# Kernel optimization log

Hardware: AMD Instinct MI355X
Metric: run time of the kernel (lower is better)

Reference implementation:

```python
import jax, jax.numpy as jnp
import numpy as np

B, S, D = 1, 2048, 1024
NH, NKV, WS = 8, 2, 64
HD = D // NH  # 128
E, HDIM, TOPK = 16, 512, 2
FP16_MIN = -65504.0
EPS = 1e-6
AUX_COEFF = 1e-5


def rmsnorm(x, w):
    return x * jax.lax.rsqrt(jnp.mean(x * x, axis=-1, keepdims=True) + EPS) * w


def setup_inputs() -> dict:
    key = jax.random.key(0)
    ks = jax.random.split(key, 24)
    r = lambda k, shape, fan: jax.random.normal(k, shape, dtype=jnp.float32) * (1.0 / np.sqrt(fan))
    return {
        "x": jax.random.normal(ks[0], (B, S, D), dtype=jnp.float32),
        "norm1_w": jnp.ones((D,), jnp.float32),
        "wq": r(ks[1], (D, NH * HD), D), "bq": jnp.zeros((NH * HD,), jnp.float32),
        "wk": r(ks[2], (D, NKV * HD), D), "bk": jnp.zeros((NKV * HD,), jnp.float32),
        "wv": r(ks[3], (D, NKV * HD), D), "bv": jnp.zeros((NKV * HD,), jnp.float32),
        "wo": r(ks[4], (NH * HD, D), NH * HD), "bo": jnp.zeros((D,), jnp.float32),
        "sink_bias": jnp.zeros((), jnp.float32),
        "norm2_w": jnp.ones((D,), jnp.float32),
        "router_w": r(ks[5], (D, E), D), "router_b": jnp.zeros((E,), jnp.float32),
        "w1": r(ks[6], (E, D, HDIM), D), "b1": jnp.zeros((E, HDIM), jnp.float32),
        "w2": r(ks[7], (E, HDIM, D), HDIM), "b2": jnp.zeros((E, D), jnp.float32),
    }


def reference(x, norm1_w, wq, bq, wk, bk, wv, bv, wo, bo, sink_bias,
              norm2_w, router_w, router_b, w1, b1, w2, b2):
    # ---- sliding-window attention with sink softmax ----
    h = rmsnorm(x, norm1_w)
    q = (h @ wq + bq).reshape(B, S, NH, HD).transpose(0, 2, 1, 3)    # [B,NH,S,HD]
    k = (h @ wk + bk).reshape(B, S, NKV, HD).transpose(0, 2, 1, 3)   # [B,NKV,S,HD]
    v = (h @ wv + bv).reshape(B, S, NKV, HD).transpose(0, 2, 1, 3)
    k = jnp.repeat(k, NH // NKV, axis=1)  # GQA expand -> [B,NH,S,HD]
    v = jnp.repeat(v, NH // NKV, axis=1)
    scores = jnp.einsum('bhqd,bhkd->bhqk', q, k) / np.sqrt(HD)
    i = jnp.arange(S)[:, None]
    j = jnp.arange(S)[None, :]
    band = (i - j >= 0) & (i - j <= WS - 1)  # causal sliding window
    scores = jnp.where(band, scores, FP16_MIN)
    m = jnp.maximum(jnp.max(scores, axis=-1, keepdims=True), sink_bias)
    ew = jnp.exp(scores - m)
    denom = jnp.sum(ew, axis=-1, keepdims=True) + jnp.exp(sink_bias - m)
    attn = ew / denom
    out = jnp.einsum('bhqk,bhkd->bhqd', attn, v).transpose(0, 2, 1, 3).reshape(B, S, D)
    x = x + (out @ wo + bo)

    # ---- MoE FFN ----
    h2 = rmsnorm(x, norm2_w)
    xf = h2.reshape(-1, D)                                  # [N,D]
    logits = (xf @ router_w + router_b) / 0.1               # [N,E]
    top_v, top_i = jax.lax.top_k(logits, TOPK)              # [N,k]
    top_w = jax.nn.softmax(top_v, axis=-1)
    probs = jax.nn.softmax(logits, axis=-1)
    aux_loss = jnp.sum(jnp.sum(probs, axis=0) ** 2) / E * AUX_COEFF
    # combine weights per (token, expert)
    gate = jnp.sum(jax.nn.one_hot(top_i, E, dtype=xf.dtype) * top_w[..., None], axis=1)  # [N,E]
    hmid = jax.nn.silu(jnp.einsum('nd,edh->neh', xf, w1) + b1)   # [N,E,H]
    y = jnp.einsum('neh,ehd->ned', hmid, w2) + b2                # [N,E,D]
    ffn = jnp.einsum('ne,ned->nd', gate, y)
    x = x + ffn.reshape(B, S, D)
    return x, aux_loss
```

## Files before the change

### kernel.cpp

```cpp
#include <hip/hip_runtime.h>
#include <hip/hip_bf16.h>

#define S     2048
#define D     1024
#define NH    8
#define NKV   2
#define HD    128
#define WS_   64
#define E_    16
#define HDIM  512
#define TOPK  2
#define NTOK  S
#define NSLOT (S*TOPK)
#define QKV_M (D + 2*NKV*HD)
#define KOFF  D
#define VOFF  (D + NKV*HD)
#define QB    8
#define WROWS (QB + WS_ - 1)
#define KPITCH 73
#define VPADF  132

typedef __attribute__((ext_vector_type(8))) short bf16x8;
typedef __attribute__((ext_vector_type(4))) float floatx4;

__device__ inline short f2bf(float f) {
    __hip_bfloat16 b = __float2bfloat16(f);
    return *reinterpret_cast<short*>(&b);
}

__global__ __launch_bounds__(256) void tconv_all(
    const float* __restrict__ wq, const float* __restrict__ wk,
    const float* __restrict__ wv, const float* __restrict__ wo,
    const float* __restrict__ w1, const float* __restrict__ w2,
    const float* __restrict__ bq, const float* __restrict__ bk,
    const float* __restrict__ bv, const float* __restrict__ router_w,
    short* __restrict__ wqkvT, short* __restrict__ woT,
    short* __restrict__ w1T, short* __restrict__ w2T,
    float* __restrict__ bqkv, float* __restrict__ rwT)
{
    int id = blockIdx.x;
    if (id >= 18950) {
        int ky = id - 18950;
        int t = threadIdx.x;
        int r = t >> 4, c = t & 15;
        int k0 = ky * 32;
        rwT[c * D + k0 + r]      = router_w[(k0 + r) * E_ + c];
        rwT[c * D + k0 + r + 16] = router_w[(k0 + r + 16) * E_ + c];
        return;
    }
    if (id >= 18944) {
        int t = (id - 18944) * 256 + threadIdx.x;
        if (t < D) bqkv[t] = bq[t];
        else if (t < VOFF) bqkv[t] = bk[t - D];
        else bqkv[t] = bv[t - VOFF];
        return;
    }
    const float* in; short* outp; int K, M, mx, ky;
    if (id < 1024)      { in = wq; outp = wqkvT;                  K = D; M = D;   int l = id;        mx = l & 31; ky = l >> 5; }
    else if (id < 1280) { in = wk; outp = wqkvT + (size_t)KOFF*D; K = D; M = 256; int l = id - 1024; mx = l & 7;  ky = l >> 3; }
    else if (id < 1536) { in = wv; outp = wqkvT + (size_t)VOFF*D; K = D; M = 256; int l = id - 1280; mx = l & 7;  ky = l >> 3; }
    else if (id < 2560) { in = wo; outp = woT;                    K = D; M = D;   int l = id - 1536; mx = l & 31; ky = l >> 5; }
    else if (id < 10752){ int l = id - 2560;  int e = l >> 9; int r = l & 511;
                          in = w1 + (size_t)e * D * HDIM; outp = w1T + (size_t)e * D * HDIM;
                          K = D; M = HDIM; mx = r & 15; ky = r >> 4; }
    else                { int l = id - 10752; int e = l >> 9; int r = l & 511;
                          in = w2 + (size_t)e * D * HDIM; outp = w2T + (size_t)e * D * HDIM;
                          K = HDIM; M = D; mx = r & 31; ky = r >> 5; }
    __shared__ float tile[32][33];
    int t = threadIdx.x, r = t >> 3, c4 = (t & 7) * 4;
    int k0 = ky * 32, m0 = mx * 32;
    float4 v = *(const float4*)&in[(size_t)(k0 + r) * M + m0 + c4];
    tile[r][c4 + 0] = v.x; tile[r][c4 + 1] = v.y;
    tile[r][c4 + 2] = v.z; tile[r][c4 + 3] = v.w;
    __syncthreads();
    short4 o;
    o.x = f2bf(tile[c4 + 0][r]);
    o.y = f2bf(tile[c4 + 1][r]);
    o.z = f2bf(tile[c4 + 2][r]);
    o.w = f2bf(tile[c4 + 3][r]);
    *(short4*)&outp[(size_t)(m0 + r) * K + k0 + c4] = o;
}

__global__ __launch_bounds__(256) void rmsnorm_kernel(
    const float* __restrict__ x, const float* __restrict__ w,
    short* __restrict__ outb)
{
    int row = blockIdx.x, t = threadIdx.x;
    float4 v = ((const float4*)(x + (size_t)row * D))[t];
    float ss = v.x*v.x + v.y*v.y + v.z*v.z + v.w*v.w;
    #pragma unroll
    for (int off = 32; off; off >>= 1) ss += __shfl_xor(ss, off, 64);
    __shared__ float red[4];
    if ((t & 63) == 0) red[t >> 6] = ss;
    __syncthreads();
    float total = red[0] + red[1] + red[2] + red[3];
    float scale = rsqrtf(total * (1.0f / (float)D) + 1e-6f);
    float4 wv = ((const float4*)w)[t];
    short4 ob;
    ob.x = f2bf(v.x * scale * wv.x); ob.y = f2bf(v.y * scale * wv.y);
    ob.z = f2bf(v.z * scale * wv.z); ob.w = f2bf(v.w * scale * wv.w);
    ((short4*)(outb + (size_t)row * D))[t] = ob;
}

template <int V, int RT>
__global__ __launch_bounds__(256) void mgemm(
    const short* __restrict__ A, const short* __restrict__ Bt,
    const float* __restrict__ bias, float* __restrict__ C,
    short* __restrict__ Cb, const float* __restrict__ res, int K, int M,
    const int* __restrict__ offs, const float* __restrict__ tok_gate)
{
    int e = (V >= 2) ? blockIdx.z : 0;
    const short* Bte = (V >= 2) ? Bt + (size_t)e * M * K : Bt;
    const float* be  = (V >= 2) ? bias + (size_t)e * M : bias;

    int row_lo, row_hi;
    if (V >= 2) {
        row_lo = offs[e] + blockIdx.y * RT;
        row_hi = offs[e + 1];
        if (row_lo >= row_hi) return;
    } else {
        row_lo = blockIdx.y * RT;
        row_hi = 1 << 30;
    }
    int col0 = blockIdx.x * 64;

    __shared__ short As[RT * 40];
    __shared__ short Bs[64 * 40];

    int t = threadIdx.x;
    int arow, ak;
    if (RT == 128) { arow = t >> 1; ak = (t & 1) * 16; }
    else           { arow = t >> 2; ak = (t & 3) * 8;  }
    int brow = t >> 2, bk = (t & 3) * 8;

    int  agrow = row_lo + arow;
    bool aval  = (V < 2) || (agrow < row_hi);
    int  asrc  = aval ? agrow : row_lo;
    const short* aptr = A   + (size_t)asrc * K + ak;
    const short* bptr = Bte + (size_t)(col0 + brow) * K + bk;
    short* as_dst = &As[arow * 40 + ak];
    short* bs_dst = &Bs[brow * 40 + bk];

    int lane = t & 63, wave = t >> 6;
    constexpr int AI = RT / 32;
    int wm = (wave & 1) * (RT / 2), wn = (wave >> 1) * 32;
    int rin = lane & 15, quad = lane >> 4;

    floatx4 acc[AI][2];
    #pragma unroll
    for (int i = 0; i < AI; ++i)
        #pragma unroll
        for (int j = 0; j < 2; ++j)
            acc[i][j] = (floatx4){0.f, 0.f, 0.f, 0.f};

    float4 a0, a1, b0;
    a0 = *(const float4*)(aptr);
    if (RT == 128) a1 = *(const float4*)(aptr + 8);
    b0 = *(const float4*)(bptr);

    for (int k0 = 0; k0 < K; k0 += 32) {
        __syncthreads();
        *(float4*)(as_dst) = a0;
        if (RT == 128) *(float4*)(as_dst + 8) = a1;
        *(float4*)(bs_dst) = b0;
        __syncthreads();
        if (k0 + 32 < K) {
            a0 = *(const float4*)(aptr + k0 + 32);
            if (RT == 128) a1 = *(const float4*)(aptr + k0 + 40);
            b0 = *(const float4*)(bptr + k0 + 32);
        }
        bf16x8 af[AI], bfr[2];
        #pragma unroll
        for (int i = 0; i < AI; ++i)
            af[i] = *(const bf16x8*)&As[(wm + i * 16 + rin) * 40 + quad * 8];
        #pragma unroll
        for (int j = 0; j < 2; ++j)
            bfr[j] = *(const bf16x8*)&Bs[(wn + j * 16 + rin) * 40 + quad * 8];
        #pragma unroll
        for (int i = 0; i < AI; ++i)
            #pragma unroll
            for (int j = 0; j < 2; ++j)
                acc[i][j] = __builtin_amdgcn_mfma_f32_16x16x32_bf16(
                    af[i], bfr[j], acc[i][j], 0, 0, 0);
    }

    #pragma unroll
    for (int i = 0; i < AI; ++i) {
        #pragma unroll
        for (int j = 0; j < 2; ++j) {
            int cg = col0 + wn + j * 16 + rin;
            #pragma unroll
            for (int rr = 0; rr < 4; ++rr) {
                int rg = row_lo + wm + i * 16 + quad * 4 + rr;
                float val = acc[i][j][rr];
                if (V == 0) {
                    C[(size_t)rg * M + cg] = val + be[cg];
                } else if (V == 1) {
                    C[(size_t)rg * M + cg] = val + be[cg] + res[(size_t)rg * M + cg];
                } else if (V == 2) {
                    if (rg < row_hi) {
                        float vb_ = val + be[cg];
                        Cb[(size_t)rg * M + cg] = f2bf(vb_ / (1.f + __expf(-vb_)));
                    }
                } else {
                    if (rg < row_hi)
                        C[(size_t)rg * M + cg] = tok_gate[rg] * (val + be[cg]);
                }
            }
        }
    }
}

__global__ __launch_bounds__(256) void attn_kernel(
    const float* __restrict__ qkv, const float* __restrict__ sink_ptr,
    short* __restrict__ ao)
{
    __shared__ __align__(16) float KT[32 * KPITCH * 4];
    __shared__ __align__(16) float Vs[WROWS * VPADF];
    __shared__ __align__(16) float Ps4[4][64][4];

    int qblk = blockIdx.x;
    int kvh  = blockIdx.y;
    int q0   = qblk * QB;
    int jbase = q0 - (WS_ - 1);

    int t = threadIdx.x;
    int c4 = (t & 31) * 4, c4g = t & 31;
    for (int r = t >> 5; r < WROWS; r += 8) {
        int j = jbase + r;
        float4 kv4 = make_float4(0.f, 0.f, 0.f, 0.f);
        float4 vv4 = make_float4(0.f, 0.f, 0.f, 0.f);
        if (j >= 0) {
            kv4 = *(const float4*)(qkv + (size_t)j * QKV_M + KOFF + kvh * HD + c4);
            vv4 = *(const float4*)(qkv + (size_t)j * QKV_M + VOFF + kvh * HD + c4);
        }
        *(float4*)&KT[(c4g * KPITCH + r) * 4] = kv4;
        *(float4*)&Vs[r * VPADF + c4] = vv4;
    }
    __syncthreads();

    int lane = t & 63, wv = t >> 6;
    float sink = sink_ptr[0];
    const float rscale = 0.08838834764831845f;

    #pragma unroll
    for (int g = 0; g < 2; ++g) {
        int qi = wv * 2 + g;
        int i  = q0 + qi;
        bool valid = (jbase + qi + lane) >= 0;

        float sc[4] = {0.f, 0.f, 0.f, 0.f};
        const float* qbase = qkv + (size_t)i * QKV_M + (kvh * 4) * HD;
        #pragma unroll
        for (int c = 0; c < 32; ++c) {
            float4 kx = *(const float4*)&KT[(c * KPITCH + qi + lane) * 4];
            #pragma unroll
            for (int hh = 0; hh < 4; ++hh) {
                float4 q4 = *(const float4*)(qbase + hh * HD + c * 4);
                sc[hh] += q4.x*kx.x + q4.y*kx.y + q4.z*kx.z + q4.w*kx.w;
            }
        }

        float pn[4];
        #pragma unroll
        for (int hh = 0; hh < 4; ++hh) {
            float s = valid ? sc[hh] * rscale : -1e30f;
            float m = s;
            #pragma unroll
            for (int off = 32; off; off >>= 1) m = fmaxf(m, __shfl_xor(m, off, 64));
            float mf = fmaxf(m, sink);
            float p  = __expf(s - mf);
            float ds = p;
            #pragma unroll
            for (int off = 32; off; off >>= 1) ds += __shfl_xor(ds, off, 64);
            pn[hh] = p / (ds + __expf(sink - mf));
        }
        *(float4*)&Ps4[wv][lane][0] = make_float4(pn[0], pn[1], pn[2], pn[3]);

        float o0=0,o1=0,o2=0,o3=0,o4=0,o5=0,o6=0,o7=0;
        const float* vp = &Vs[qi * VPADF + 2 * lane];
        #pragma unroll
        for (int jj = 0; jj < 64; ++jj) {
            float4 p4 = *(const float4*)&Ps4[wv][jj][0];
            float2 vv = *(const float2*)(vp + jj * VPADF);
            o0 += p4.x * vv.x; o1 += p4.x * vv.y;
            o2 += p4.y * vv.x; o3 += p4.y * vv.y;
            o4 += p4.z * vv.x; o5 += p4.z * vv.y;
            o6 += p4.w * vv.x; o7 += p4.w * vv.y;
        }
        short2 r0; r0.x = f2bf(o0); r0.y = f2bf(o1);
        short2 r1; r1.x = f2bf(o2); r1.y = f2bf(o3);
        short2 r2; r2.x = f2bf(o4); r2.y = f2bf(o5);
        short2 r3; r3.x = f2bf(o6); r3.y = f2bf(o7);
        ((short2*)(ao + (size_t)i * D + (kvh * 4 + 0) * HD))[lane] = r0;
        ((short2*)(ao + (size_t)i * D + (kvh * 4 + 1) * HD))[lane] = r1;
        ((short2*)(ao + (size_t)i * D + (kvh * 4 + 2) * HD))[lane] = r2;
        ((short2*)(ao + (size_t)i * D + (kvh * 4 + 3) * HD))[lane] = r3;
    }
}

__global__ __launch_bounds__(256) void rms_router_kernel(
    const float* __restrict__ x1, const float* __restrict__ w,
    short* __restrict__ h2b, const float* __restrict__ rwT,
    const float* __restrict__ rb, float* __restrict__ probs,
    int* __restrict__ top_i, float* __restrict__ top_g)
{
    int tok = blockIdx.x, t = threadIdx.x;
    __shared__ float hrow[D];
    float4 v = ((const float4*)(x1 + (size_t)tok * D))[t];
    float ss = v.x*v.x + v.y*v.y + v.z*v.z + v.w*v.w;
    #pragma unroll
    for (int off = 32; off; off >>= 1) ss += __shfl_xor(ss, off, 64);
    __shared__ float red[4];
    if ((t & 63) == 0) red[t >> 6] = ss;
    __syncthreads();
    float total = red[0] + red[1] + red[2] + red[3];
    float scale = rsqrtf(total * (1.0f / (float)D) + 1e-6f);
    float4 wv = ((const float4*)w)[t];
    float4 o;
    o.x = v.x * scale * wv.x; o.y = v.y * scale * wv.y;
    o.z = v.z * scale * wv.z; o.w = v.w * scale * wv.w;
    ((float4*)hrow)[t] = o;
    short4 ob;
    ob.x = f2bf(o.x); ob.y = f2bf(o.y); ob.z = f2bf(o.z); ob.w = f2bf(o.w);
    ((short4*)(h2b + (size_t)tok * D))[t] = ob;
    __syncthreads();

    int e = t & 15, seg = t >> 4;
    const float4* rwp = (const float4*)(rwT + (size_t)e * D + seg * 64);
    const float4* hp  = (const float4*)(hrow + seg * 64);
    float part = 0.f;
    #pragma unroll
    for (int i = 0; i < 16; ++i) {
        float4 a = hp[i];
        float4 b = rwp[i];
        part += a.x * b.x; part += a.y * b.y;
        part += a.z * b.z; part += a.w * b.w;
    }
    __shared__ float lpart[256];
    lpart[t] = part;
    __syncthreads();
    __shared__ float logits[E_];
    if (t < E_) {
        float sl = 0.f;
        for (int sg = 0; sg < 16; ++sg) sl += lpart[sg * 16 + t];
        logits[t] = (sl + rb[t]) * 10.0f;
    }
    __syncthreads();
    __shared__ float sm[2];
    if (t == 0) {
        float mx = logits[0];
        for (int x = 1; x < E_; ++x) mx = fmaxf(mx, logits[x]);
        float ps = 0.f;
        for (int x = 0; x < E_; ++x) ps += __expf(logits[x] - mx);
        sm[0] = mx; sm[1] = ps;
        int i0 = 0; float v0 = logits[0];
        for (int x = 1; x < E_; ++x) if (logits[x] > v0) { v0 = logits[x]; i0 = x; }
        int i1 = -1; float v1 = -3.4e38f;
        for (int x = 0; x < E_; ++x) {
            if (x == i0) continue;
            if (logits[x] > v1) { v1 = logits[x]; i1 = x; }
        }
        float e1 = __expf(v1 - v0);
        float g0 = 1.f / (1.f + e1);
        float g1 = e1 * g0;
        top_i[tok * 2 + 0] = i0; top_g[tok * 2 + 0] = g0;
        top_i[tok * 2 + 1] = i1; top_g[tok * 2 + 1] = g1;
    }
    __syncthreads();
    if (t < E_) probs[tok * E_ + t] = __expf(logits[t] - sm[0]) / sm[1];
}

__global__ __launch_bounds__(256) void finalize_kernel(
    const float* __restrict__ probs, const int* __restrict__ top_i,
    int* __restrict__ offs, int* __restrict__ cursor,
    float* __restrict__ aux_out)
{
    __shared__ float csum[E_];
    __shared__ int hist[E_];
    int t = threadIdx.x;
    if (t < E_) { csum[t] = 0.f; hist[t] = 0; }
    __syncthreads();

    int c = t & 15, g = t >> 4;
    float part = 0.f;
    for (int i = 0; i < NTOK / 16; ++i)
        part += probs[(size_t)(i * 16 + g) * E_ + c];
    atomicAdd(&csum[c], part);

    int h = 0;
    for (int i = 0; i < NSLOT / 256; ++i) {
        int eidx = top_i[i * 256 + t];
        atomicAdd(&hist[eidx], 1);
    }
    (void)h;
    __syncthreads();

    if (t == 0) {
        int acc = 0;
        for (int e = 0; e < E_; ++e) { offs[e] = acc; cursor[e] = acc; acc += hist[e]; }
        offs[E_] = acc;
        float s = 0.f;
        for (int e = 0; e < E_; ++e) s += csum[e] * csum[e];
        *aux_out = s / (float)E_ * 1e-5f;
    }
}

__global__ __launch_bounds__(256) void scatter_kernel(
    const int* __restrict__ top_i, const float* __restrict__ top_g,
    int* __restrict__ cursor, int* __restrict__ tok_idx,
    float* __restrict__ tok_gate, int* __restrict__ slot_of)
{
    int tok = blockIdx.x * 256 + threadIdx.x;
    if (tok >= NTOK) return;
    for (int s = 0; s < TOPK; ++s) {
        int e = top_i[tok * 2 + s];
        int pos = atomicAdd(&cursor[e], 1);
        tok_idx[pos]  = tok;
        tok_gate[pos] = top_g[tok * 2 + s];
        slot_of[tok * 2 + s] = pos;
    }
}

__global__ __launch_bounds__(256) void gather_kernel(
    const short* __restrict__ h2b, const int* __restrict__ tok_idx,
    short* __restrict__ xg)
{
    int slot = blockIdx.x * 2 + (threadIdx.x >> 7);
    int c = (threadIdx.x & 127) * 8;
    int tok = tok_idx[slot];
    *(float4*)&xg[(size_t)slot * D + c] =
        *(const float4*)&h2b[(size_t)tok * D + c];
}

__global__ __launch_bounds__(256) void combine_kernel(
    const float* __restrict__ x1, const float* __restrict__ y,
    const int* __restrict__ slot_of, float* __restrict__ out)
{
    int tok = blockIdx.x, t = threadIdx.x;
    int s0 = slot_of[tok * 2], s1 = slot_of[tok * 2 + 1];
    float4 a = ((const float4*)(x1 + (size_t)tok * D))[t];
    float4 b = ((const float4*)(y + (size_t)s0 * D))[t];
    float4 c = ((const float4*)(y + (size_t)s1 * D))[t];
    float4 o;
    o.x = a.x + b.x + c.x; o.y = a.y + b.y + c.y;
    o.z = a.z + b.z + c.z; o.w = a.w + b.w + c.w;
    ((float4*)(out + (size_t)tok * D))[t] = o;
}

extern "C" void kernel_launch(void* const* d_in, const int* in_sizes, int n_in,
                              void* d_out, int out_size, void* d_ws, size_t ws_size,
                              hipStream_t stream)
{
    const float* x        = (const float*)d_in[0];
    const float* norm1_w  = (const float*)d_in[1];
    const float* wq       = (const float*)d_in[2];
    const float* bq       = (const float*)d_in[3];
    const float* wk       = (const float*)d_in[4];
    const float* bk       = (const float*)d_in[5];
    const float* wv       = (const float*)d_in[6];
    const float* bv       = (const float*)d_in[7];
    const float* wo       = (const float*)d_in[8];
    const float* bo       = (const float*)d_in[9];
    const float* sink     = (const float*)d_in[10];
    const float* norm2_w  = (const float*)d_in[11];
    const float* router_w = (const float*)d_in[12];
    const float* router_b = (const float*)d_in[13];
    const float* w1       = (const float*)d_in[14];
    const float* b1       = (const float*)d_in[15];
    const float* w2       = (const float*)d_in[16];
    const float* b2       = (const float*)d_in[17];
    float* out = (float*)d_out;

    char* w = (char*)d_ws;
    auto alloc = [&](size_t bytes) {
        char* p = w; w += (bytes + 255) & ~255ull; return p;
    };
    short* wqkvT = (short*)alloc((size_t)QKV_M * D * 2);
    short* woT   = (short*)alloc((size_t)D * D * 2);
    short* w1T   = (short*)alloc((size_t)E_ * HDIM * D * 2);
    short* w2T   = (short*)alloc((size_t)E_ * D * HDIM * 2);
    float* bqkv  = (float*)alloc(QKV_M * 4);
    float* rwT   = (float*)alloc((size_t)E_ * D * 4);
    short* h_bf  = (short*)alloc((size_t)S * D * 2);
    float* qkv   = (float*)alloc((size_t)S * QKV_M * 4);
    float* x1    = (float*)alloc((size_t)S * D * 4);
    short* h2b   = (short*)alloc((size_t)S * D * 2);
    short* xg    = (short*)alloc((size_t)NSLOT * D * 2);
    float* yslot = (float*)alloc((size_t)NSLOT * D * 4);
    float* probs = (float*)alloc((size_t)NTOK * E_ * 4);
    int*   offs     = (int*)alloc(17 * 4);
    int*   cursor   = (int*)alloc(16 * 4);
    int*   top_i    = (int*)alloc((size_t)NSLOT * 4);
    float* top_g    = (float*)alloc((size_t)NSLOT * 4);
    int*   tok_idx  = (int*)alloc((size_t)NSLOT * 4);
    float* tok_gate = (float*)alloc((size_t)NSLOT * 4);
    int*   slot_of  = (int*)alloc((size_t)NSLOT * 4);
    short* ao_bf = h_bf;
    short* hmid  = (short*)qkv;

    tconv_all<<<18982, 256, 0, stream>>>(wq, wk, wv, wo, w1, w2, bq, bk, bv,
                                         router_w, wqkvT, woT, w1T, w2T,
                                         bqkv, rwT);

    rmsnorm_kernel<<<S, 256, 0, stream>>>(x, norm1_w, h_bf);

    mgemm<0, 128><<<dim3(QKV_M / 64, S / 128), 256, 0, stream>>>(
        h_bf, wqkvT, bqkv, qkv, nullptr, nullptr, D, QKV_M, nullptr, nullptr);

    attn_kernel<<<dim3(S / QB, NKV), 256, 0, stream>>>(qkv, sink, ao_bf);

    mgemm<1, 128><<<dim3(D / 64, S / 128), 256, 0, stream>>>(
        ao_bf, woT, bo, x1, nullptr, x, D, D, nullptr, nullptr);

    rms_router_kernel<<<NTOK, 256, 0, stream>>>(x1, norm2_w, h2b, rwT,
                                                router_b, probs, top_i, top_g);

    finalize_kernel<<<1, 256, 0, stream>>>(probs, top_i, offs, cursor,
                                           out + (size_t)S * D);

    scatter_kernel<<<(NTOK + 255) / 256, 256, 0, stream>>>(
        top_i, top_g, cursor, tok_idx, tok_gate, slot_of);

    gather_kernel<<<NSLOT / 2, 256, 0, stream>>>(h2b, tok_idx, xg);

    mgemm<2, 64><<<dim3(HDIM / 64, 32, E_), 256, 0, stream>>>(
        xg, w1T, b1, nullptr, hmid, nullptr, D, HDIM, offs, nullptr);

    mgemm<3, 64><<<dim3(D / 64, 32, E_), 256, 0, stream>>>(
        hmid, w2T, b2, yslot, nullptr, nullptr, HDIM, D, offs, tok_gate);

    combine_kernel<<<NTOK, 256, 0, stream>>>(x1, yslot, slot_of, out);
}
```

Baseline: 329.8 us.

## Double-buffer GEMM LDS with 64-wide K steps and uniform 64-row tiles

Rewrites the shared bf16 MFMA GEMM to take K in steps of 64, split into two 32-wide sub-tiles, with double-buffered LDS. The next tile is staged while the current one is computed, which drops to one barrier per iteration instead of two. The dense QKV and output-projection GEMMs move from 128-row to 64-row tiles, doubling their block count. The MoE grouped GEMMs launch up to 64 row tiles per expert (NSLOT/64) instead of 32, so heavily loaded experts get full coverage. It also masks routing indices and seeds the second top-k search from a real logit, which guards against out-of-range indices but adds a few ALU ops. LDS use per block grows and the per-block work for the dense GEMMs shrinks.

```diff
diff --git a/kernel.cpp b/kernel.cpp
--- a/kernel.cpp
+++ b/kernel.cpp
@@ -102,7 +102,7 @@
     ((short4*)(outb + (size_t)row * D))[t] = ob;
 }
 
-template <int V, int RT>
+template <int V>
 __global__ __launch_bounds__(256) void mgemm(
     const short* __restrict__ A, const short* __restrict__ Bt,
     const float* __restrict__ bias, float* __restrict__ C,
@@ -115,77 +115,101 @@
 
     int row_lo, row_hi;
     if (V >= 2) {
-        row_lo = offs[e] + blockIdx.y * RT;
+        row_lo = offs[e] + blockIdx.y * 64;
         row_hi = offs[e + 1];
         if (row_lo >= row_hi) return;
     } else {
-        row_lo = blockIdx.y * RT;
+        row_lo = blockIdx.y * 64;
         row_hi = 1 << 30;
     }
     int col0 = blockIdx.x * 64;
 
-    __shared__ short As[RT * 40];
-    __shared__ short Bs[64 * 40];
+    constexpr int SUB = 64 * 40;
+    constexpr int BUF = 2 * SUB;
+    __shared__ short As[2 * BUF];
+    __shared__ short Bs[2 * BUF];
 
     int t = threadIdx.x;
-    int arow, ak;
-    if (RT == 128) { arow = t >> 1; ak = (t & 1) * 16; }
-    else           { arow = t >> 2; ak = (t & 3) * 8;  }
-    int brow = t >> 2, bk = (t & 3) * 8;
-
-    int  agrow = row_lo + arow;
+    int srow = t >> 2;
+    int skq  = t & 3;
+    int sgk  = skq * 16;
+    int ssub = skq >> 1;
+    int soff = (skq & 1) * 16;
+
+    int  agrow = row_lo + srow;
     bool aval  = (V < 2) || (agrow < row_hi);
     int  asrc  = aval ? agrow : row_lo;
-    const short* aptr = A   + (size_t)asrc * K + ak;
-    const short* bptr = Bte + (size_t)(col0 + brow) * K + bk;
-    short* as_dst = &As[arow * 40 + ak];
-    short* bs_dst = &Bs[brow * 40 + bk];
+    const short* aptr = A   + (size_t)asrc * K + sgk;
+    const short* bptr = Bte + (size_t)(col0 + srow) * K + sgk;
+    short* as_w = &As[ssub * SUB + srow * 40 + soff];
+    short* bs_w = &Bs[ssub * SUB + srow * 40 + soff];
 
     int lane = t & 63, wave = t >> 6;
-    constexpr int AI = RT / 32;
-    int wm = (wave & 1) * (RT / 2), wn = (wave >> 1) * 32;
+    int wm = (wave & 1) * 32, wn = (wave >> 1) * 32;
     int rin = lane & 15, quad = lane >> 4;
 
-    floatx4 acc[AI][2];
+    floatx4 acc[2][2];
     #pragma unroll
-    for (int i = 0; i < AI; ++i)
+    for (int i = 0; i < 2; ++i)
         #pragma unroll
         for (int j = 0; j < 2; ++j)
             acc[i][j] = (floatx4){0.f, 0.f, 0.f, 0.f};
 
-    float4 a0, a1, b0;
-    a0 = *(const float4*)(aptr);
-    if (RT == 128) a1 = *(const float4*)(aptr + 8);
-    b0 = *(const float4*)(bptr);
-
-    for (int k0 = 0; k0 < K; k0 += 32) {
+    float4 va0 = *(const float4*)(aptr);
+    float4 va1 = *(const float4*)(aptr + 8);
+    float4 vb0 = *(const float4*)(bptr);
+    float4 vb1 = *(const float4*)(bptr + 8);
+    *(float4*)(as_w)     = va0;
+    *(float4*)(as_w + 8) = va1;
+    *(float4*)(bs_w)     = vb0;
+    *(float4*)(bs_w + 8) = vb1;
+    if (K > 64) {
+        va0 = *(const float4*)(aptr + 64);
+        va1 = *(const float4*)(aptr + 72);
+        vb0 = *(const float4*)(bptr + 64);
+        vb1 = *(const float4*)(bptr + 72);
+    }
+    __syncthreads();
+
+    const int NIT = K >> 6;
+    for (int it = 0; it < NIT; ++it) {
+        int cur = it & 1, nxt = cur ^ 1;
+        if (it + 1 < NIT) {
+            *(float4*)(as_w + nxt * BUF)     = va0;
+            *(float4*)(as_w + nxt * BUF + 8) = va1;
+            *(float4*)(bs_w + nxt * BUF)     = vb0;
+            *(float4*)(bs_w + nxt * BUF + 8) = vb1;
+            if (it + 2 < NIT) {
+                int k2 = (it + 2) << 6;
+                va0 = *(const float4*)(aptr + k2);
+                va1 = *(const float4*)(aptr + k2 + 8);
+                vb0 = *(const float4*)(bptr + k2);
+                vb1 = *(const float4*)(bptr + k2 + 8);
+            }
+        }
+        #pragma unroll
+        for (int s = 0; s < 2; ++s) {
+            bf16x8 af[2], bfr[2];
+            #pragma unroll
+            for (int i = 0; i < 2; ++i)
+                af[i] = *(const bf16x8*)&As[cur * BUF + s * SUB
+                                            + (wm + i * 16 + rin) * 40 + quad * 8];
+            #pragma unroll
+            for (int j = 0; j < 2; ++j)
+                bfr[j] = *(const bf16x8*)&Bs[cur * BUF + s * SUB
+                                             + (wn + j * 16 + rin) * 40 + quad * 8];
+            #pragma unroll
+            for (int i = 0; i < 2; ++i)
+                #pragma unroll
+                for (int j = 0; j < 2; ++j)
+                    acc[i][j] = __builtin_amdgcn_mfma_f32_16x16x32_bf16(
+                        af[i], bfr[j], acc[i][j], 0, 0, 0);
+        }
         __syncthreads();
-        *(float4*)(as_dst) = a0;
-        if (RT == 128) *(float4*)(as_dst + 8) = a1;
-        *(float4*)(bs_dst) = b0;
-        __syncthreads();
-        if (k0 + 32 < K) {
-            a0 = *(const float4*)(aptr + k0 + 32);
-            if (RT == 128) a1 = *(const float4*)(aptr + k0 + 40);
-            b0 = *(const float4*)(bptr + k0 + 32);
-        }
-        bf16x8 af[AI], bfr[2];
-        #pragma unroll
-        for (int i = 0; i < AI; ++i)
-            af[i] = *(const bf16x8*)&As[(wm + i * 16 + rin) * 40 + quad * 8];
-        #pragma unroll
-        for (int j = 0; j < 2; ++j)
-            bfr[j] = *(const bf16x8*)&Bs[(wn + j * 16 + rin) * 40 + quad * 8];
-        #pragma unroll
-        for (int i = 0; i < AI; ++i)
-            #pragma unroll
-            for (int j = 0; j < 2; ++j)
-                acc[i][j] = __builtin_amdgcn_mfma_f32_16x16x32_bf16(
-                    af[i], bfr[j], acc[i][j], 0, 0, 0);
     }
 
     #pragma unroll
-    for (int i = 0; i < AI; ++i) {
+    for (int i = 0; i < 2; ++i) {
         #pragma unroll
         for (int j = 0; j < 2; ++j) {
             int cg = col0 + wn + j * 16 + rin;
@@ -356,7 +380,7 @@
         sm[0] = mx; sm[1] = ps;
         int i0 = 0; float v0 = logits[0];
         for (int x = 1; x < E_; ++x) if (logits[x] > v0) { v0 = logits[x]; i0 = x; }
-        int i1 = -1; float v1 = -3.4e38f;
+        int i1 = (i0 == 0) ? 1 : 0; float v1 = logits[i1];
         for (int x = 0; x < E_; ++x) {
             if (x == i0) continue;
             if (logits[x] > v1) { v1 = logits[x]; i1 = x; }
@@ -388,12 +412,10 @@
         part += probs[(size_t)(i * 16 + g) * E_ + c];
     atomicAdd(&csum[c], part);
 
-    int h = 0;
     for (int i = 0; i < NSLOT / 256; ++i) {
-        int eidx = top_i[i * 256 + t];
+        int eidx = top_i[i * 256 + t] & 15;
         atomicAdd(&hist[eidx], 1);
     }
-    (void)h;
     __syncthreads();
 
     if (t == 0) {
@@ -414,8 +436,8 @@
     int tok = blockIdx.x * 256 + threadIdx.x;
     if (tok >= NTOK) return;
     for (int s = 0; s < TOPK; ++s) {
-        int e = top_i[tok * 2 + s];
-        int pos = atomicAdd(&cursor[e], 1);
+        int e = top_i[tok * 2 + s] & 15;
+        int pos = atomicAdd(&cursor[e], 1) & (NSLOT - 1);
         tok_idx[pos]  = tok;
         tok_gate[pos] = top_g[tok * 2 + s];
         slot_of[tok * 2 + s] = pos;
@@ -428,7 +450,7 @@
 {
     int slot = blockIdx.x * 2 + (threadIdx.x >> 7);
     int c = (threadIdx.x & 127) * 8;
-    int tok = tok_idx[slot];
+    int tok = tok_idx[slot] & (NTOK - 1);
     *(float4*)&xg[(size_t)slot * D + c] =
         *(const float4*)&h2b[(size_t)tok * D + c];
 }
@@ -438,7 +460,7 @@
     const int* __restrict__ slot_of, float* __restrict__ out)
 {
     int tok = blockIdx.x, t = threadIdx.x;
-    int s0 = slot_of[tok * 2], s1 = slot_of[tok * 2 + 1];
+    int s0 = slot_of[tok * 2] & (NSLOT - 1), s1 = slot_of[tok * 2 + 1] & (NSLOT - 1);
     float4 a = ((const float4*)(x1 + (size_t)tok * D))[t];
     float4 b = ((const float4*)(y + (size_t)s0 * D))[t];
     float4 c = ((const float4*)(y + (size_t)s1 * D))[t];
@@ -505,12 +527,12 @@
 
     rmsnorm_kernel<<<S, 256, 0, stream>>>(x, norm1_w, h_bf);
 
-    mgemm<0, 128><<<dim3(QKV_M / 64, S / 128), 256, 0, stream>>>(
+    mgemm<0><<<dim3(QKV_M / 64, S / 64), 256, 0, stream>>>(
         h_bf, wqkvT, bqkv, qkv, nullptr, nullptr, D, QKV_M, nullptr, nullptr);
 
     attn_kernel<<<dim3(S / QB, NKV), 256, 0, stream>>>(qkv, sink, ao_bf);
 
-    mgemm<1, 128><<<dim3(D / 64, S / 128), 256, 0, stream>>>(
+    mgemm<1><<<dim3(D / 64, S / 64), 256, 0, stream>>>(
         ao_bf, woT, bo, x1, nullptr, x, D, D, nullptr, nullptr);
 
     rms_router_kernel<<<NTOK, 256, 0, stream>>>(x1, norm2_w, h2b, rwT,
@@ -524,10 +546,10 @@
 
     gather_kernel<<<NSLOT / 2, 256, 0, stream>>>(h2b, tok_idx, xg);
 
-    mgemm<2, 64><<<dim3(HDIM / 64, 32, E_), 256, 0, stream>>>(
+    mgemm<2><<<dim3(HDIM / 64, NSLOT / 64, E_), 256, 0, stream>>>(
         xg, w1T, b1, nullptr, hmid, nullptr, D, HDIM, offs, nullptr);
 
-    mgemm<3, 64><<<dim3(D / 64, 32, E_), 256, 0, stream>>>(
+    mgemm<3><<<dim3(D / 64, NSLOT / 64, E_), 256, 0, stream>>>(
         hmid, w2T, b2, yslot, nullptr, nullptr, HDIM, D, offs, tok_gate);
 
     combine_kernel<<<NTOK, 256, 0, stream>>>(x1, yslot, slot_of, out);
```

New measurement: 297.3 us. -9.9%, faster.
